# Kernel tuning notes

Hardware: AMD Instinct MI355X
Metric: run time of the kernel (lower is better)

Reference implementation:

```python
import jax, jax.numpy as jnp
import numpy as np

N = 100000   # nodes
E = 5000000  # edges (avg degree 50)
H = 16       # hidden dim


def gcn_conv(x, edge_index, edge_weight, W, b, num_nodes):
    """PyG GCNConv with edge weights: add self-loops (weight 1), symmetric
    normalization deg^-1/2 * w * deg^-1/2, linear transform, scatter-add."""
    row, col = edge_index[0], edge_index[1]  # source j -> target i
    loop = jnp.arange(num_nodes, dtype=edge_index.dtype)
    row = jnp.concatenate([row, loop])
    col = jnp.concatenate([col, loop])
    w = jnp.concatenate([edge_weight, jnp.ones((num_nodes,), edge_weight.dtype)])
    deg = jax.ops.segment_sum(w, col, num_segments=num_nodes)
    dinv = jnp.where(deg > 0, jax.lax.rsqrt(jnp.where(deg > 0, deg, 1.0)), 0.0)
    norm = dinv[row] * w * dinv[col]               # [E+N]
    h = x @ W                                      # [N, out]
    msg = norm[:, None] * h[row]                   # gather + scale
    out = jax.ops.segment_sum(msg, col, num_segments=num_nodes)  # scatter-add
    return out + b


def setup_inputs() -> dict:
    key = jax.random.key(0)
    k = jax.random.split(key, 7)
    x = jax.random.normal(k[0], (N, 1), dtype=jnp.float32)
    edge_index = jax.random.randint(k[1], (2, E), 0, N, dtype=jnp.int32)
    edge_attr = jax.random.uniform(k[2], (E,), dtype=jnp.float32)
    W1 = jax.random.normal(k[3], (1, H), dtype=jnp.float32) * (1.0 / np.sqrt(1.0))
    b1 = jnp.zeros((H,), dtype=jnp.float32)
    W2 = jax.random.normal(k[4], (H, 1), dtype=jnp.float32) * (1.0 / np.sqrt(H))
    b2 = jnp.zeros((1,), dtype=jnp.float32)
    return {"x": x, "edge_index": edge_index, "edge_attr": edge_attr,
            "W1": W1, "b1": b1, "W2": W2, "b2": b2}


def reference(x, edge_index, edge_attr, W1, b1, W2, b2):
    h = gcn_conv(x, edge_index, edge_attr, W1, b1, N)
    h = jax.nn.relu(h)
    out = gcn_conv(h, edge_index, edge_attr, W2, b2, N)
    return out
```

## Files before the change

kernel.cpp:

```cpp
#include <hip/hip_runtime.h>

#define T       256
#define BSHIFT  12
#define BSIZE   4096
#define MAXNB   32
#define M       32
#define EPB     4096
#define EPT     (EPB / T)
#define HSTRIDE 260

__global__ void k_count(const int* __restrict__ col, int* __restrict__ cntT,
                        int E, int nb, int ebp) {
    __shared__ unsigned short hist[MAXNB][HSTRIDE];
    int t = threadIdx.x, g = blockIdx.x, lane = t & 63, wid = t >> 6;
    for (int b = 0; b < nb; ++b) hist[b][t] = 0;
    __syncthreads();
    int base = g * EPB;
    bool full = (base + EPB <= E);
    if (full) {
#pragma unroll
        for (int k = 0; k < EPT / 4; ++k) {
            int4 c = *(const int4*)(col + base + (t + k * T) * 4);
            ++hist[c.x >> BSHIFT][t];
            ++hist[c.y >> BSHIFT][t];
            ++hist[c.z >> BSHIFT][t];
            ++hist[c.w >> BSHIFT][t];
        }
    } else {
        for (int k = 0; k < EPT; ++k) {
            int e = base + t + k * T;
            if (e < E) ++hist[col[e] >> BSHIFT][t];
        }
    }
    __syncthreads();
    for (int b = wid; b < nb; b += 4) {
        const unsigned short* hp = &hist[b][lane * 4];
        int s = (int)hp[0] + hp[1] + hp[2] + hp[3];
#pragma unroll
        for (int d = 32; d >= 1; d >>= 1) s += __shfl_xor(s, d, 64);
        if (lane == 0) cntT[b * ebp + g] = s;
    }
}

__global__ void k_scan(const int* __restrict__ cntT, int* __restrict__ ofsT,
                       int* __restrict__ tot, int eb, int ebp) {
    __shared__ int wsum[4];
    __shared__ int carry;
    int b = blockIdx.x, t = threadIdx.x, lane = t & 63, wid = t >> 6;
    if (t == 0) carry = 0;
    __syncthreads();
    int rounds = (eb + T - 1) / T;
    for (int jr = 0; jr < rounds; ++jr) {
        int idx = jr * T + t;
        int v = (idx < eb) ? cntT[b * ebp + idx] : 0;
        int inc = v;
#pragma unroll
        for (int d = 1; d < 64; d <<= 1) {
            int o = __shfl_up(inc, d, 64);
            if (lane >= d) inc += o;
        }
        if (lane == 63) wsum[wid] = inc;
        __syncthreads();
        int add = carry;
        for (int w = 0; w < wid; ++w) add += wsum[w];
        if (idx < eb) ofsT[b * ebp + idx] = inc - v + add;
        __syncthreads();
        if (t == 0) carry += wsum[0] + wsum[1] + wsum[2] + wsum[3];
        __syncthreads();
    }
    if (t == 0) tot[b] = carry;
}

__global__ void k_scatter(const int* __restrict__ row, const int* __restrict__ col,
                          const float* __restrict__ w,
                          const int* __restrict__ cntT, const int* __restrict__ ofsT,
                          const int* __restrict__ tot,
                          int2* __restrict__ rec, int E, int nb, int ebp) {
    __shared__ unsigned short cur[MAXNB][HSTRIDE];
    __shared__ int  lofs[MAXNB + 1];
    __shared__ int  btot[MAXNB];
    __shared__ int  rbase[MAXNB];
    __shared__ int2 buf[EPB];
    int t = threadIdx.x, g = blockIdx.x, lane = t & 63, wid = t >> 6;
    for (int b = 0; b < nb; ++b) cur[b][t] = 0;
    __syncthreads();

    int base = g * EPB;
    bool full = (base + EPB <= E);
    int4 c0, c1, c2, c3;
    if (full) {
        c0 = *(const int4*)(col + base + (t + 0 * T) * 4);
        c1 = *(const int4*)(col + base + (t + 1 * T) * 4);
        c2 = *(const int4*)(col + base + (t + 2 * T) * 4);
        c3 = *(const int4*)(col + base + (t + 3 * T) * 4);
        ++cur[c0.x >> BSHIFT][t]; ++cur[c0.y >> BSHIFT][t];
        ++cur[c0.z >> BSHIFT][t]; ++cur[c0.w >> BSHIFT][t];
        ++cur[c1.x >> BSHIFT][t]; ++cur[c1.y >> BSHIFT][t];
        ++cur[c1.z >> BSHIFT][t]; ++cur[c1.w >> BSHIFT][t];
        ++cur[c2.x >> BSHIFT][t]; ++cur[c2.y >> BSHIFT][t];
        ++cur[c2.z >> BSHIFT][t]; ++cur[c2.w >> BSHIFT][t];
        ++cur[c3.x >> BSHIFT][t]; ++cur[c3.y >> BSHIFT][t];
        ++cur[c3.z >> BSHIFT][t]; ++cur[c3.w >> BSHIFT][t];
    } else {
        for (int k = 0; k < EPT; ++k) {
            int e = base + t + k * T;
            if (e < E) ++cur[col[e] >> BSHIFT][t];
        }
    }
    __syncthreads();

    for (int b = wid; b < nb; b += 4) {
        unsigned short* hp = &cur[b][lane * 4];
        int a0 = hp[0], a1 = hp[1], a2 = hp[2], a3 = hp[3];
        int tsum = a0 + a1 + a2 + a3;
        int inc = tsum;
#pragma unroll
        for (int d = 1; d < 64; d <<= 1) {
            int o = __shfl_up(inc, d, 64);
            if (lane >= d) inc += o;
        }
        int excl = inc - tsum;
        hp[0] = (unsigned short)excl;
        hp[1] = (unsigned short)(excl + a0);
        hp[2] = (unsigned short)(excl + a0 + a1);
        hp[3] = (unsigned short)(excl + a0 + a1 + a2);
        if (lane == 63) btot[b] = inc;
    }
    __syncthreads();

    if (t < 64) {
        int tv = (t < nb) ? ((tot[t] + 3) & ~3) : 0;
        int incA = tv;
#pragma unroll
        for (int d = 1; d < 32; d <<= 1) {
            int o = __shfl_up(incA, d, 64);
            if (t >= d) incA += o;
        }
        int h = (t < nb) ? btot[t] : 0;
        int incB = h;
#pragma unroll
        for (int d = 1; d < 32; d <<= 1) {
            int o = __shfl_up(incB, d, 64);
            if (t >= d) incB += o;
        }
        if (t == 0) lofs[0] = 0;
        if (t < nb) {
            lofs[t + 1] = incB;
            rbase[t] = (incA - tv) + ofsT[t * ebp + g];
        }
    }
    __syncthreads();

    auto place = [&](int c, int r, float wv) {
        int bb = c >> BSHIFT;
        int o = cur[bb][t];
        cur[bb][t] = (unsigned short)(o + 1);
        int pos = lofs[bb] + o;
        buf[pos] = make_int2(((c & (BSIZE - 1)) << 17) | r, __float_as_int(wv));
    };
    if (full) {
        {
            int idx = base + (t + 0 * T) * 4;
            int4 r = *(const int4*)(row + idx);
            float4 wv = *(const float4*)(w + idx);
            place(c0.x, r.x, wv.x); place(c0.y, r.y, wv.y);
            place(c0.z, r.z, wv.z); place(c0.w, r.w, wv.w);
        }
        {
            int idx = base + (t + 1 * T) * 4;
            int4 r = *(const int4*)(row + idx);
            float4 wv = *(const float4*)(w + idx);
            place(c1.x, r.x, wv.x); place(c1.y, r.y, wv.y);
            place(c1.z, r.z, wv.z); place(c1.w, r.w, wv.w);
        }
        {
            int idx = base + (t + 2 * T) * 4;
            int4 r = *(const int4*)(row + idx);
            float4 wv = *(const float4*)(w + idx);
            place(c2.x, r.x, wv.x); place(c2.y, r.y, wv.y);
            place(c2.z, r.z, wv.z); place(c2.w, r.w, wv.w);
        }
        {
            int idx = base + (t + 3 * T) * 4;
            int4 r = *(const int4*)(row + idx);
            float4 wv = *(const float4*)(w + idx);
            place(c3.x, r.x, wv.x); place(c3.y, r.y, wv.y);
            place(c3.z, r.z, wv.z); place(c3.w, r.w, wv.w);
        }
    } else {
        for (int k = 0; k < EPT; ++k) {
            int e = base + t + k * T;
            if (e < E) {
                int c = col[e];
                place(c, row[e], w[e]);
            }
        }
    }
    __syncthreads();

    int total = lofs[nb];
    int b = 0;
    for (int j = t; j < total; j += T) {
        while (j >= lofs[b + 1]) ++b;
        rec[rbase[b] + (j - lofs[b])] = buf[j];
    }
}

template <bool HAS_SRC>
__global__ void k_acc(const int2* __restrict__ rec, const int* __restrict__ tot,
                      const float* __restrict__ src, float* __restrict__ part, int nb) {
    __shared__ float acc[BSIZE];
    __shared__ int   bst[MAXNB];
    int t = threadIdx.x, g = blockIdx.x;
    int b = g / M, m = g % M;
    if (t < 64) {
        int tv = (t < nb) ? ((tot[t] + 3) & ~3) : 0;
        int inc = tv;
#pragma unroll
        for (int d = 1; d < 32; d <<= 1) {
            int o = __shfl_up(inc, d, 64);
            if (t >= d) inc += o;
        }
        if (t < nb) bst[t] = inc - tv;
    }
    for (int j = t; j < BSIZE; j += T) acc[j] = 0.0f;
    __syncthreads();
    int s  = bst[b];
    int tb = tot[b];
    int chunk = ((tb + M - 1) / M + 7) & ~7;
    int lo = s + m * chunk;
    int hi = min(s + tb, lo + chunk);
    const int4* rec4 = (const int4*)rec;
    int i = lo + t * 8;
    for (; i + 7 < hi; i += T * 8) {
        int4 q0 = rec4[(i >> 1) + 0];
        int4 q1 = rec4[(i >> 1) + 1];
        int4 q2 = rec4[(i >> 1) + 2];
        int4 q3 = rec4[(i >> 1) + 3];
        float v0 = __int_as_float(q0.y), v1 = __int_as_float(q0.w);
        float v2 = __int_as_float(q1.y), v3 = __int_as_float(q1.w);
        float v4 = __int_as_float(q2.y), v5 = __int_as_float(q2.w);
        float v6 = __int_as_float(q3.y), v7 = __int_as_float(q3.w);
        if (HAS_SRC) {
            v0 *= src[q0.x & 0x1FFFF]; v1 *= src[q0.z & 0x1FFFF];
            v2 *= src[q1.x & 0x1FFFF]; v3 *= src[q1.z & 0x1FFFF];
            v4 *= src[q2.x & 0x1FFFF]; v5 *= src[q2.z & 0x1FFFF];
            v6 *= src[q3.x & 0x1FFFF]; v7 *= src[q3.z & 0x1FFFF];
        }
        atomicAdd(&acc[((unsigned)q0.x) >> 17], v0);
        atomicAdd(&acc[((unsigned)q0.z) >> 17], v1);
        atomicAdd(&acc[((unsigned)q1.x) >> 17], v2);
        atomicAdd(&acc[((unsigned)q1.z) >> 17], v3);
        atomicAdd(&acc[((unsigned)q2.x) >> 17], v4);
        atomicAdd(&acc[((unsigned)q2.z) >> 17], v5);
        atomicAdd(&acc[((unsigned)q3.x) >> 17], v6);
        atomicAdd(&acc[((unsigned)q3.z) >> 17], v7);
    }
    for (; i < hi; ++i) {
        int2 r = rec[i];
        float v = __int_as_float(r.y);
        if (HAS_SRC) v *= src[r.x & 0x1FFFF];
        atomicAdd(&acc[((unsigned)r.x) >> 17], v);
    }
    __syncthreads();
    float* dst = part + (size_t)g * BSIZE;
    for (int j = t; j < BSIZE; j += T) dst[j] = acc[j];
}

__device__ __forceinline__ float reduceM(const float* __restrict__ part, int n) {
    int b = n >> BSHIFT, o = n & (BSIZE - 1);
    const float* pp = part + (size_t)b * M * BSIZE + o;
    float s = 0.0f;
#pragma unroll
    for (int m = 0; m < M; ++m) s += pp[(size_t)m * BSIZE];
    return s;
}

__global__ void k_red_dinv(const float* __restrict__ part, const float* __restrict__ x,
                           float* __restrict__ dinv, float* __restrict__ p, int N) {
    int i = blockIdx.x * blockDim.x + threadIdx.x;
    if (i < N) {
        float d  = reduceM(part, i) + 1.0f;
        float di = rsqrtf(d);
        dinv[i] = di;
        p[i] = di * x[i];
    }
}

__global__ void k_red_mlp(const float* __restrict__ part, const float* __restrict__ dinv,
                          const float* __restrict__ p,
                          const float* __restrict__ W1, const float* __restrict__ b1,
                          const float* __restrict__ W2,
                          float* __restrict__ q, int N) {
    int i = blockIdx.x * blockDim.x + threadIdx.x;
    if (i < N) {
        float di = dinv[i];
        float s  = di * reduceM(part, i) + di * p[i];
        float acc = 0.0f;
#pragma unroll
        for (int k = 0; k < 16; ++k) {
            float h = fmaxf(s * W1[k] + b1[k], 0.0f);
            acc += h * W2[k];
        }
        q[i] = di * acc;
    }
}

__global__ void k_red_out(const float* __restrict__ part, const float* __restrict__ dinv,
                          const float* __restrict__ q, const float* __restrict__ b2,
                          float* __restrict__ out, int N) {
    int i = blockIdx.x * blockDim.x + threadIdx.x;
    if (i < N) {
        float di = dinv[i];
        out[i] = di * reduceM(part, i) + di * q[i] + b2[0];
    }
}

extern "C" void kernel_launch(void* const* d_in, const int* in_sizes, int n_in,
                              void* d_out, int out_size, void* d_ws, size_t ws_size,
                              hipStream_t stream) {
    const float* x  = (const float*)d_in[0];
    const int*   ei = (const int*)  d_in[1];
    const float* ew = (const float*)d_in[2];
    const float* W1 = (const float*)d_in[3];
    const float* b1 = (const float*)d_in[4];
    const float* W2 = (const float*)d_in[5];
    const float* b2 = (const float*)d_in[6];

    const int N = in_sizes[0];
    const int E = in_sizes[2];
    const int* row = ei;
    const int* col = ei + E;
    const int nb  = (N + BSIZE - 1) >> BSHIFT;
    const int eb  = (E + EPB - 1) / EPB;
    const int ebp = (eb + 63) & ~63;

    char* wsp = (char*)d_ws;
    auto take = [&](size_t bytes) {
        char* r = wsp; wsp += (bytes + 255) & ~(size_t)255; return (void*)r;
    };
    int2*  rec  = (int2*) take((size_t)(E + 4 * MAXNB) * 8);
    float* part = (float*)take((size_t)nb * M * BSIZE * 4);
    float* dinv = (float*)take((size_t)N * 4);
    float* p    = (float*)take((size_t)N * 4);
    float* q    = (float*)take((size_t)N * 4);
    int*   cntT = (int*)  take((size_t)MAXNB * ebp * 4);
    int*   ofsT = (int*)  take((size_t)MAXNB * ebp * 4);
    int*   tot  = (int*)  take(MAXNB * 4);

    float* out = (float*)d_out;

    const int nbk = (N + T - 1) / T;
    const int ab  = nb * M;

    k_count  <<<eb, T, 0, stream>>>(col, cntT, E, nb, ebp);
    k_scan   <<<nb, T, 0, stream>>>(cntT, ofsT, tot, eb, ebp);
    k_scatter<<<eb, T, 0, stream>>>(row, col, ew, cntT, ofsT, tot, rec, E, nb, ebp);

    k_acc<false><<<ab, T, 0, stream>>>(rec, tot, nullptr, part, nb);
    k_red_dinv  <<<nbk, T, 0, stream>>>(part, x, dinv, p, N);

    k_acc<true><<<ab, T, 0, stream>>>(rec, tot, p, part, nb);
    k_red_mlp  <<<nbk, T, 0, stream>>>(part, dinv, p, W1, b1, W2, q, N);

    k_acc<true><<<ab, T, 0, stream>>>(rec, tot, q, part, nb);
    k_red_out  <<<nbk, T, 0, stream>>>(part, dinv, q, b2, out, N);
}
```

Baseline: 251.0 us.

## Fuse all GCN phases into one persistent cooperative kernel with grid syncs

Replaces the nine separate launches (count, scan, scatter, three accumulate and three reduce kernels) with a single cooperative kernel that loops over work and separates phases with grid.sync. The count/scan prepass is removed: each edge block builds a small shared histogram with atomics and reserves space in fixed-capacity per-bucket regions through global atomicAdd on gcnt. This removes launch overhead and the extra pass over col, at the cost of nondeterministic record ordering and a fixed per-bucket capacity (CAP) that could overflow on skewed inputs.

```diff
diff --git a/kernel.cpp b/kernel.cpp
--- a/kernel.cpp
+++ b/kernel.cpp
@@ -1,318 +1,221 @@
 #include <hip/hip_runtime.h>
+#include <hip/hip_cooperative_groups.h>
+
+namespace cg = cooperative_groups;
 
 #define T       256
 #define BSHIFT  12
 #define BSIZE   4096
 #define MAXNB   32
-#define M       32
+#define MM      32
 #define EPB     4096
 #define EPT     (EPB / T)
-#define HSTRIDE 260
-
-__global__ void k_count(const int* __restrict__ col, int* __restrict__ cntT,
-                        int E, int nb, int ebp) {
-    __shared__ unsigned short hist[MAXNB][HSTRIDE];
-    int t = threadIdx.x, g = blockIdx.x, lane = t & 63, wid = t >> 6;
-    for (int b = 0; b < nb; ++b) hist[b][t] = 0;
-    __syncthreads();
-    int base = g * EPB;
-    bool full = (base + EPB <= E);
-    if (full) {
+#define CAP     212992
+
+__global__ __launch_bounds__(T, 4) void k_all(
+        const int* __restrict__ row, const int* __restrict__ col,
+        const float* __restrict__ w, const float* __restrict__ x,
+        const float* __restrict__ W1, const float* __restrict__ b1,
+        const float* __restrict__ W2, const float* __restrict__ b2,
+        int2* __restrict__ rec, float* __restrict__ part,
+        float* __restrict__ dinv, float* __restrict__ p, float* __restrict__ q,
+        int* __restrict__ gcnt, float* __restrict__ out,
+        int E, int N, int nb, int eb) {
+    cg::grid_group grid = cg::this_grid();
+
+    __shared__ int2 buf[EPB];
+    __shared__ int  rnk[MAXNB];
+    __shared__ int  lofs[MAXNB + 1];
+    __shared__ int  rbase[MAXNB];
+    float* acc = (float*)buf;
+
+    const int t = threadIdx.x;
+
+    for (int g = blockIdx.x; g < eb; g += gridDim.x) {
+        if (t < MAXNB) rnk[t] = 0;
+        __syncthreads();
+        int base = g * EPB;
+        bool full = (base + EPB <= E);
+        int4 c0, c1, c2, c3;
+        if (full) {
+            c0 = *(const int4*)(col + base + (t + 0 * T) * 4);
+            c1 = *(const int4*)(col + base + (t + 1 * T) * 4);
+            c2 = *(const int4*)(col + base + (t + 2 * T) * 4);
+            c3 = *(const int4*)(col + base + (t + 3 * T) * 4);
+            atomicAdd(&rnk[c0.x >> BSHIFT], 1); atomicAdd(&rnk[c0.y >> BSHIFT], 1);
+            atomicAdd(&rnk[c0.z >> BSHIFT], 1); atomicAdd(&rnk[c0.w >> BSHIFT], 1);
+            atomicAdd(&rnk[c1.x >> BSHIFT], 1); atomicAdd(&rnk[c1.y >> BSHIFT], 1);
+            atomicAdd(&rnk[c1.z >> BSHIFT], 1); atomicAdd(&rnk[c1.w >> BSHIFT], 1);
+            atomicAdd(&rnk[c2.x >> BSHIFT], 1); atomicAdd(&rnk[c2.y >> BSHIFT], 1);
+            atomicAdd(&rnk[c2.z >> BSHIFT], 1); atomicAdd(&rnk[c2.w >> BSHIFT], 1);
+            atomicAdd(&rnk[c3.x >> BSHIFT], 1); atomicAdd(&rnk[c3.y >> BSHIFT], 1);
+            atomicAdd(&rnk[c3.z >> BSHIFT], 1); atomicAdd(&rnk[c3.w >> BSHIFT], 1);
+        } else {
+            for (int k = 0; k < EPT; ++k) {
+                int e = base + t + k * T;
+                if (e < E) atomicAdd(&rnk[col[e] >> BSHIFT], 1);
+            }
+        }
+        __syncthreads();
+        if (t < 64) {
+            int v = (t < nb) ? rnk[t] : 0;
+            int inc = v;
 #pragma unroll
-        for (int k = 0; k < EPT / 4; ++k) {
-            int4 c = *(const int4*)(col + base + (t + k * T) * 4);
-            ++hist[c.x >> BSHIFT][t];
-            ++hist[c.y >> BSHIFT][t];
-            ++hist[c.z >> BSHIFT][t];
-            ++hist[c.w >> BSHIFT][t];
-        }
-    } else {
-        for (int k = 0; k < EPT; ++k) {
-            int e = base + t + k * T;
-            if (e < E) ++hist[col[e] >> BSHIFT][t];
-        }
-    }
-    __syncthreads();
-    for (int b = wid; b < nb; b += 4) {
-        const unsigned short* hp = &hist[b][lane * 4];
-        int s = (int)hp[0] + hp[1] + hp[2] + hp[3];
+            for (int d = 1; d < 32; d <<= 1) {
+                int o = __shfl_up(inc, d, 64);
+                if (t >= d) inc += o;
+            }
+            if (t == 0) lofs[0] = 0;
+            if (t < nb) {
+                lofs[t + 1] = inc;
+                rbase[t] = t * CAP + atomicAdd(&gcnt[t], v);
+            }
+        }
+        __syncthreads();
+        if (t < MAXNB) rnk[t] = 0;
+        __syncthreads();
+        auto place = [&](int c, int r, float wv) {
+            int b = c >> BSHIFT;
+            int pos = lofs[b] + atomicAdd(&rnk[b], 1);
+            buf[pos] = make_int2(((c & (BSIZE - 1)) << 17) | r, __float_as_int(wv));
+        };
+        if (full) {
+            {
+                int idx = base + (t + 0 * T) * 4;
+                int4 r = *(const int4*)(row + idx);
+                float4 wv = *(const float4*)(w + idx);
+                place(c0.x, r.x, wv.x); place(c0.y, r.y, wv.y);
+                place(c0.z, r.z, wv.z); place(c0.w, r.w, wv.w);
+            }
+            {
+                int idx = base + (t + 1 * T) * 4;
+                int4 r = *(const int4*)(row + idx);
+                float4 wv = *(const float4*)(w + idx);
+                place(c1.x, r.x, wv.x); place(c1.y, r.y, wv.y);
+                place(c1.z, r.z, wv.z); place(c1.w, r.w, wv.w);
+            }
+            {
+                int idx = base + (t + 2 * T) * 4;
+                int4 r = *(const int4*)(row + idx);
+                float4 wv = *(const float4*)(w + idx);
+                place(c2.x, r.x, wv.x); place(c2.y, r.y, wv.y);
+                place(c2.z, r.z, wv.z); place(c2.w, r.w, wv.w);
+            }
+            {
+                int idx = base + (t + 3 * T) * 4;
+                int4 r = *(const int4*)(row + idx);
+                float4 wv = *(const float4*)(w + idx);
+                place(c3.x, r.x, wv.x); place(c3.y, r.y, wv.y);
+                place(c3.z, r.z, wv.z); place(c3.w, r.w, wv.w);
+            }
+        } else {
+            for (int k = 0; k < EPT; ++k) {
+                int e = base + t + k * T;
+                if (e < E) place(col[e], row[e], w[e]);
+            }
+        }
+        __syncthreads();
+        int total = lofs[nb];
+        int b = 0;
+        for (int j = t; j < total; j += T) {
+            while (j >= lofs[b + 1]) ++b;
+            rec[rbase[b] + (j - lofs[b])] = buf[j];
+        }
+        __syncthreads();
+    }
+    grid.sync();
+
+    auto acc_phase = [&](const float* __restrict__ src, bool has_src) {
+        for (int s = blockIdx.x; s < nb * MM; s += gridDim.x) {
+            int b = s / MM, m = s % MM;
+            for (int j = t; j < BSIZE; j += T) acc[j] = 0.0f;
+            __syncthreads();
+            int s0 = b * CAP;
+            int tb = gcnt[b];
+            int chunk = ((tb + MM - 1) / MM + 7) & ~7;
+            int lo = s0 + m * chunk;
+            int hi = min(s0 + tb, lo + chunk);
+            const int4* rec4 = (const int4*)rec;
+            int i = lo + t * 8;
+            for (; i + 7 < hi; i += T * 8) {
+                int4 q0 = rec4[(i >> 1) + 0];
+                int4 q1 = rec4[(i >> 1) + 1];
+                int4 q2 = rec4[(i >> 1) + 2];
+                int4 q3 = rec4[(i >> 1) + 3];
+                float v0 = __int_as_float(q0.y), v1 = __int_as_float(q0.w);
+                float v2 = __int_as_float(q1.y), v3 = __int_as_float(q1.w);
+                float v4 = __int_as_float(q2.y), v5 = __int_as_float(q2.w);
+                float v6 = __int_as_float(q3.y), v7 = __int_as_float(q3.w);
+                if (has_src) {
+                    v0 *= src[q0.x & 0x1FFFF]; v1 *= src[q0.z & 0x1FFFF];
+                    v2 *= src[q1.x & 0x1FFFF]; v3 *= src[q1.z & 0x1FFFF];
+                    v4 *= src[q2.x & 0x1FFFF]; v5 *= src[q2.z & 0x1FFFF];
+                    v6 *= src[q3.x & 0x1FFFF]; v7 *= src[q3.z & 0x1FFFF];
+                }
+                atomicAdd(&acc[((unsigned)q0.x) >> 17], v0);
+                atomicAdd(&acc[((unsigned)q0.z) >> 17], v1);
+                atomicAdd(&acc[((unsigned)q1.x) >> 17], v2);
+                atomicAdd(&acc[((unsigned)q1.z) >> 17], v3);
+                atomicAdd(&acc[((unsigned)q2.x) >> 17], v4);
+                atomicAdd(&acc[((unsigned)q2.z) >> 17], v5);
+                atomicAdd(&acc[((unsigned)q3.x) >> 17], v6);
+                atomicAdd(&acc[((unsigned)q3.z) >> 17], v7);
+            }
+            for (; i < hi; ++i) {
+                int2 r = rec[i];
+                float v = __int_as_float(r.y);
+                if (has_src) v *= src[r.x & 0x1FFFF];
+                atomicAdd(&acc[((unsigned)r.x) >> 17], v);
+            }
+            __syncthreads();
+            float* dst = part + (size_t)s * BSIZE;
+            for (int j = t; j < BSIZE; j += T) dst[j] = acc[j];
+            __syncthreads();
+        }
+    };
+
+    auto reduceM = [&](int n) {
+        int b = n >> BSHIFT, o = n & (BSIZE - 1);
+        const float* pp = part + (size_t)b * MM * BSIZE + o;
+        float sum = 0.0f;
 #pragma unroll
-        for (int d = 32; d >= 1; d >>= 1) s += __shfl_xor(s, d, 64);
-        if (lane == 0) cntT[b * ebp + g] = s;
-    }
-}
-
-__global__ void k_scan(const int* __restrict__ cntT, int* __restrict__ ofsT,
-                       int* __restrict__ tot, int eb, int ebp) {
-    __shared__ int wsum[4];
-    __shared__ int carry;
-    int b = blockIdx.x, t = threadIdx.x, lane = t & 63, wid = t >> 6;
-    if (t == 0) carry = 0;
-    __syncthreads();
-    int rounds = (eb + T - 1) / T;
-    for (int jr = 0; jr < rounds; ++jr) {
-        int idx = jr * T + t;
-        int v = (idx < eb) ? cntT[b * ebp + idx] : 0;
-        int inc = v;
-#pragma unroll
-        for (int d = 1; d < 64; d <<= 1) {
-            int o = __shfl_up(inc, d, 64);
-            if (lane >= d) inc += o;
-        }
-        if (lane == 63) wsum[wid] = inc;
-        __syncthreads();
-        int add = carry;
-        for (int w = 0; w < wid; ++w) add += wsum[w];
-        if (idx < eb) ofsT[b * ebp + idx] = inc - v + add;
-        __syncthreads();
-        if (t == 0) carry += wsum[0] + wsum[1] + wsum[2] + wsum[3];
-        __syncthreads();
-    }
-    if (t == 0) tot[b] = carry;
-}
-
-__global__ void k_scatter(const int* __restrict__ row, const int* __restrict__ col,
-                          const float* __restrict__ w,
-                          const int* __restrict__ cntT, const int* __restrict__ ofsT,
-                          const int* __restrict__ tot,
-                          int2* __restrict__ rec, int E, int nb, int ebp) {
-    __shared__ unsigned short cur[MAXNB][HSTRIDE];
-    __shared__ int  lofs[MAXNB + 1];
-    __shared__ int  btot[MAXNB];
-    __shared__ int  rbase[MAXNB];
-    __shared__ int2 buf[EPB];
-    int t = threadIdx.x, g = blockIdx.x, lane = t & 63, wid = t >> 6;
-    for (int b = 0; b < nb; ++b) cur[b][t] = 0;
-    __syncthreads();
-
-    int base = g * EPB;
-    bool full = (base + EPB <= E);
-    int4 c0, c1, c2, c3;
-    if (full) {
-        c0 = *(const int4*)(col + base + (t + 0 * T) * 4);
-        c1 = *(const int4*)(col + base + (t + 1 * T) * 4);
-        c2 = *(const int4*)(col + base + (t + 2 * T) * 4);
-        c3 = *(const int4*)(col + base + (t + 3 * T) * 4);
-        ++cur[c0.x >> BSHIFT][t]; ++cur[c0.y >> BSHIFT][t];
-        ++cur[c0.z >> BSHIFT][t]; ++cur[c0.w >> BSHIFT][t];
-        ++cur[c1.x >> BSHIFT][t]; ++cur[c1.y >> BSHIFT][t];
-        ++cur[c1.z >> BSHIFT][t]; ++cur[c1.w >> BSHIFT][t];
-        ++cur[c2.x >> BSHIFT][t]; ++cur[c2.y >> BSHIFT][t];
-        ++cur[c2.z >> BSHIFT][t]; ++cur[c2.w >> BSHIFT][t];
-        ++cur[c3.x >> BSHIFT][t]; ++cur[c3.y >> BSHIFT][t];
-        ++cur[c3.z >> BSHIFT][t]; ++cur[c3.w >> BSHIFT][t];
-    } else {
-        for (int k = 0; k < EPT; ++k) {
-            int e = base + t + k * T;
-            if (e < E) ++cur[col[e] >> BSHIFT][t];
-        }
-    }
-    __syncthreads();
-
-    for (int b = wid; b < nb; b += 4) {
-        unsigned short* hp = &cur[b][lane * 4];
-        int a0 = hp[0], a1 = hp[1], a2 = hp[2], a3 = hp[3];
-        int tsum = a0 + a1 + a2 + a3;
-        int inc = tsum;
-#pragma unroll
-        for (int d = 1; d < 64; d <<= 1) {
-            int o = __shfl_up(inc, d, 64);
-            if (lane >= d) inc += o;
-        }
-        int excl = inc - tsum;
-        hp[0] = (unsigned short)excl;
-        hp[1] = (unsigned short)(excl + a0);
-        hp[2] = (unsigned short)(excl + a0 + a1);
-        hp[3] = (unsigned short)(excl + a0 + a1 + a2);
-        if (lane == 63) btot[b] = inc;
-    }
-    __syncthreads();
-
-    if (t < 64) {
-        int tv = (t < nb) ? ((tot[t] + 3) & ~3) : 0;
-        int incA = tv;
-#pragma unroll
-        for (int d = 1; d < 32; d <<= 1) {
-            int o = __shfl_up(incA, d, 64);
-            if (t >= d) incA += o;
-        }
-        int h = (t < nb) ? btot[t] : 0;
-        int incB = h;
-#pragma unroll
-        for (int d = 1; d < 32; d <<= 1) {
-            int o = __shfl_up(incB, d, 64);
-            if (t >= d) incB += o;
-        }
-        if (t == 0) lofs[0] = 0;
-        if (t < nb) {
-            lofs[t + 1] = incB;
-            rbase[t] = (incA - tv) + ofsT[t * ebp + g];
-        }
-    }
-    __syncthreads();
-
-    auto place = [&](int c, int r, float wv) {
-        int bb = c >> BSHIFT;
-        int o = cur[bb][t];
-        cur[bb][t] = (unsigned short)(o + 1);
-        int pos = lofs[bb] + o;
-        buf[pos] = make_int2(((c & (BSIZE - 1)) << 17) | r, __float_as_int(wv));
-    };
-    if (full) {
-        {
-            int idx = base + (t + 0 * T) * 4;
-            int4 r = *(const int4*)(row + idx);
-            float4 wv = *(const float4*)(w + idx);
-            place(c0.x, r.x, wv.x); place(c0.y, r.y, wv.y);
-            place(c0.z, r.z, wv.z); place(c0.w, r.w, wv.w);
-        }
-        {
-            int idx = base + (t + 1 * T) * 4;
-            int4 r = *(const int4*)(row + idx);
-            float4 wv = *(const float4*)(w + idx);
-            place(c1.x, r.x, wv.x); place(c1.y, r.y, wv.y);
-            place(c1.z, r.z, wv.z); place(c1.w, r.w, wv.w);
-        }
-        {
-            int idx = base + (t + 2 * T) * 4;
-            int4 r = *(const int4*)(row + idx);
-            float4 wv = *(const float4*)(w + idx);
-            place(c2.x, r.x, wv.x); place(c2.y, r.y, wv.y);
-            place(c2.z, r.z, wv.z); place(c2.w, r.w, wv.w);
-        }
-        {
-            int idx = base + (t + 3 * T) * 4;
-            int4 r = *(const int4*)(row + idx);
-            float4 wv = *(const float4*)(w + idx);
-            place(c3.x, r.x, wv.x); place(c3.y, r.y, wv.y);
-            place(c3.z, r.z, wv.z); place(c3.w, r.w, wv.w);
-        }
-    } else {
-        for (int k = 0; k < EPT; ++k) {
-            int e = base + t + k * T;
-            if (e < E) {
-                int c = col[e];
-                place(c, row[e], w[e]);
-            }
-        }
-    }
-    __syncthreads();
-
-    int total = lofs[nb];
-    int b = 0;
-    for (int j = t; j < total; j += T) {
-        while (j >= lofs[b + 1]) ++b;
-        rec[rbase[b] + (j - lofs[b])] = buf[j];
-    }
-}
-
-template <bool HAS_SRC>
-__global__ void k_acc(const int2* __restrict__ rec, const int* __restrict__ tot,
-                      const float* __restrict__ src, float* __restrict__ part, int nb) {
-    __shared__ float acc[BSIZE];
-    __shared__ int   bst[MAXNB];
-    int t = threadIdx.x, g = blockIdx.x;
-    int b = g / M, m = g % M;
-    if (t < 64) {
-        int tv = (t < nb) ? ((tot[t] + 3) & ~3) : 0;
-        int inc = tv;
-#pragma unroll
-        for (int d = 1; d < 32; d <<= 1) {
-            int o = __shfl_up(inc, d, 64);
-            if (t >= d) inc += o;
-        }
-        if (t < nb) bst[t] = inc - tv;
-    }
-    for (int j = t; j < BSIZE; j += T) acc[j] = 0.0f;
-    __syncthreads();
-    int s  = bst[b];
-    int tb = tot[b];
-    int chunk = ((tb + M - 1) / M + 7) & ~7;
-    int lo = s + m * chunk;
-    int hi = min(s + tb, lo + chunk);
-    const int4* rec4 = (const int4*)rec;
-    int i = lo + t * 8;
-    for (; i + 7 < hi; i += T * 8) {
-        int4 q0 = rec4[(i >> 1) + 0];
-        int4 q1 = rec4[(i >> 1) + 1];
-        int4 q2 = rec4[(i >> 1) + 2];
-        int4 q3 = rec4[(i >> 1) + 3];
-        float v0 = __int_as_float(q0.y), v1 = __int_as_float(q0.w);
-        float v2 = __int_as_float(q1.y), v3 = __int_as_float(q1.w);
-        float v4 = __int_as_float(q2.y), v5 = __int_as_float(q2.w);
-        float v6 = __int_as_float(q3.y), v7 = __int_as_float(q3.w);
-        if (HAS_SRC) {
-            v0 *= src[q0.x & 0x1FFFF]; v1 *= src[q0.z & 0x1FFFF];
-            v2 *= src[q1.x & 0x1FFFF]; v3 *= src[q1.z & 0x1FFFF];
-            v4 *= src[q2.x & 0x1FFFF]; v5 *= src[q2.z & 0x1FFFF];
-            v6 *= src[q3.x & 0x1FFFF]; v7 *= src[q3.z & 0x1FFFF];
-        }
-        atomicAdd(&acc[((unsigned)q0.x) >> 17], v0);
-        atomicAdd(&acc[((unsigned)q0.z) >> 17], v1);
-        atomicAdd(&acc[((unsigned)q1.x) >> 17], v2);
-        atomicAdd(&acc[((unsigned)q1.z) >> 17], v3);
-        atomicAdd(&acc[((unsigned)q2.x) >> 17], v4);
-        atomicAdd(&acc[((unsigned)q2.z) >> 17], v5);
-        atomicAdd(&acc[((unsigned)q3.x) >> 17], v6);
-        atomicAdd(&acc[((unsigned)q3.z) >> 17], v7);
-    }
-    for (; i < hi; ++i) {
-        int2 r = rec[i];
-        float v = __int_as_float(r.y);
-        if (HAS_SRC) v *= src[r.x & 0x1FFFF];
-        atomicAdd(&acc[((unsigned)r.x) >> 17], v);
-    }
-    __syncthreads();
-    float* dst = part + (size_t)g * BSIZE;
-    for (int j = t; j < BSIZE; j += T) dst[j] = acc[j];
-}
-
-__device__ __forceinline__ float reduceM(const float* __restrict__ part, int n) {
-    int b = n >> BSHIFT, o = n & (BSIZE - 1);
-    const float* pp = part + (size_t)b * M * BSIZE + o;
-    float s = 0.0f;
-#pragma unroll
-    for (int m = 0; m < M; ++m) s += pp[(size_t)m * BSIZE];
-    return s;
-}
-
-__global__ void k_red_dinv(const float* __restrict__ part, const float* __restrict__ x,
-                           float* __restrict__ dinv, float* __restrict__ p, int N) {
-    int i = blockIdx.x * blockDim.x + threadIdx.x;
-    if (i < N) {
-        float d  = reduceM(part, i) + 1.0f;
+        for (int m = 0; m < MM; ++m) sum += pp[(size_t)m * BSIZE];
+        return sum;
+    };
+
+    acc_phase(nullptr, false);
+    grid.sync();
+
+    for (int i = blockIdx.x * T + t; i < N; i += gridDim.x * T) {
+        float d  = reduceM(i) + 1.0f;
         float di = rsqrtf(d);
         dinv[i] = di;
         p[i] = di * x[i];
     }
-}
-
-__global__ void k_red_mlp(const float* __restrict__ part, const float* __restrict__ dinv,
-                          const float* __restrict__ p,
-                          const float* __restrict__ W1, const float* __restrict__ b1,
-                          const float* __restrict__ W2,
-                          float* __restrict__ q, int N) {
-    int i = blockIdx.x * blockDim.x + threadIdx.x;
-    if (i < N) {
+    grid.sync();
+
+    acc_phase(p, true);
+    grid.sync();
+
+    for (int i = blockIdx.x * T + t; i < N; i += gridDim.x * T) {
         float di = dinv[i];
-        float s  = di * reduceM(part, i) + di * p[i];
-        float acc = 0.0f;
+        float s  = di * reduceM(i) + di * p[i];
+        float a = 0.0f;
 #pragma unroll
         for (int k = 0; k < 16; ++k) {
             float h = fmaxf(s * W1[k] + b1[k], 0.0f);
-            acc += h * W2[k];
-        }
-        q[i] = di * acc;
-    }
-}
-
-__global__ void k_red_out(const float* __restrict__ part, const float* __restrict__ dinv,
-                          const float* __restrict__ q, const float* __restrict__ b2,
-                          float* __restrict__ out, int N) {
-    int i = blockIdx.x * blockDim.x + threadIdx.x;
-    if (i < N) {
+            a += h * W2[k];
+        }
+        q[i] = di * a;
+    }
+    grid.sync();
+
+    acc_phase(q, true);
+    grid.sync();
+
+    for (int i = blockIdx.x * T + t; i < N; i += gridDim.x * T) {
         float di = dinv[i];
-        out[i] = di * reduceM(part, i) + di * q[i] + b2[0];
+        out[i] = di * reduceM(i) + di * q[i] + b2[0];
     }
 }
 
@@ -327,42 +230,50 @@
     const float* W2 = (const float*)d_in[5];
     const float* b2 = (const float*)d_in[6];
 
-    const int N = in_sizes[0];
-    const int E = in_sizes[2];
+    int N = in_sizes[0];
+    int E = in_sizes[2];
     const int* row = ei;
     const int* col = ei + E;
-    const int nb  = (N + BSIZE - 1) >> BSHIFT;
-    const int eb  = (E + EPB - 1) / EPB;
-    const int ebp = (eb + 63) & ~63;
+    int nb = (N + BSIZE - 1) >> BSHIFT;
+    int eb = (E + EPB - 1) / EPB;
 
     char* wsp = (char*)d_ws;
     auto take = [&](size_t bytes) {
         char* r = wsp; wsp += (bytes + 255) & ~(size_t)255; return (void*)r;
     };
-    int2*  rec  = (int2*) take((size_t)(E + 4 * MAXNB) * 8);
-    float* part = (float*)take((size_t)nb * M * BSIZE * 4);
+    int2*  rec  = (int2*) take((size_t)nb * CAP * 8);
+    float* part = (float*)take((size_t)nb * MM * BSIZE * 4);
     float* dinv = (float*)take((size_t)N * 4);
     float* p    = (float*)take((size_t)N * 4);
     float* q    = (float*)take((size_t)N * 4);
-    int*   cntT = (int*)  take((size_t)MAXNB * ebp * 4);
-    int*   ofsT = (int*)  take((size_t)MAXNB * ebp * 4);
-    int*   tot  = (int*)  take(MAXNB * 4);
+    int*   gcnt = (int*)  take(MAXNB * 4);
 
     float* out = (float*)d_out;
 
-    const int nbk = (N + T - 1) / T;
-    const int ab  = nb * M;
-
-    k_count  <<<eb, T, 0, stream>>>(col, cntT, E, nb, ebp);
-    k_scan   <<<nb, T, 0, stream>>>(cntT, ofsT, tot, eb, ebp);
-    k_scatter<<<eb, T, 0, stream>>>(row, col, ew, cntT, ofsT, tot, rec, E, nb, ebp);
-
-    k_acc<false><<<ab, T, 0, stream>>>(rec, tot, nullptr, part, nb);
-    k_red_dinv  <<<nbk, T, 0, stream>>>(part, x, dinv, p, N);
-
-    k_acc<true><<<ab, T, 0, stream>>>(rec, tot, p, part, nb);
-    k_red_mlp  <<<nbk, T, 0, stream>>>(part, dinv, p, W1, b1, W2, q, N);
-
-    k_acc<true><<<ab, T, 0, stream>>>(rec, tot, q, part, nb);
-    k_red_out  <<<nbk, T, 0, stream>>>(part, dinv, q, b2, out, N);
+    static int grid_blocks = 0;
+    if (grid_blocks == 0) {
+        int occ = 0;
+        (void)hipOccupancyMaxActiveBlocksPerMultiprocessor(&occ, (const void*)k_all, T, 0);
+        if (occ < 1) occ = 1;
+        hipDeviceProp_t props;
+        int dev = 0;
+        (void)hipGetDevice(&dev);
+        (void)hipGetDeviceProperties(&props, dev);
+        int cap = occ * props.multiProcessorCount;
+        int want = nb * MM;
+        grid_blocks = cap < want ? cap : want;
+        if (grid_blocks < 1) grid_blocks = 1;
+    }
+
+    (void)hipMemsetAsync(gcnt, 0, MAXNB * sizeof(int), stream);
+
+    void* args[] = {
+        (void*)&row, (void*)&col, (void*)&ew, (void*)&x,
+        (void*)&W1, (void*)&b1, (void*)&W2, (void*)&b2,
+        (void*)&rec, (void*)&part, (void*)&dinv, (void*)&p, (void*)&q,
+        (void*)&gcnt, (void*)&out,
+        (void*)&E, (void*)&N, (void*)&nb, (void*)&eb
+    };
+    (void)hipLaunchCooperativeKernel((const void*)k_all, dim3(grid_blocks), dim3(T),
+                                     args, 0, stream);
 }
```

Result: slower. 777.9 us (+209.9%).
